# Optimization experiments

Measured on AMD Instinct MI355X. Metric: run time of the kernel, lower is better.

The kernel has to match this reference:

```python
import jax, jax.numpy as jnp
import numpy as np

N, S, T = 32, 256, 256
ENC, H, MEL, PRE, DIN, PN = 512, 256, 80, 128, 64, 512


def setup_inputs():
    key = jax.random.key(0)
    ks = iter(jax.random.split(key, 64))
    def rn(shape, s=0.05):
        return jax.random.normal(next(ks), shape, dtype=jnp.float32) * s
    return dict(
        encoder_outputs=rn((N, S, ENC), 1.0),
        mels=rn((N, MEL, T), 1.0),
        text_lengths=jax.random.randint(next(ks), (N,), 1, S),
        output_lengths=jax.random.randint(next(ks), (N,), 1, T),
        tf_ratio=0,
        enc_Wih=rn((2, 2, 4 * H, ENC)), enc_Whh=rn((2, 2, 4 * H, H)), enc_b=rn((2, 2, 4 * H)),
        Wk=rn((512, 512, 9)), bk=rn((512,)), Wv=rn((512, 512, 9)), bv=rn((512,)),
        Wq=rn((512, 64, 24)), bq=rn((512,)),
        initial_context=rn((1, 1, MEL), 1.0),
        pre_W1=rn((PRE, MEL), 0.1), pre_b1=rn((PRE,)), pre_s1=jnp.ones(PRE, jnp.float32),
        pre_W2=rn((PRE, PRE), 0.1), pre_b2=rn((PRE,)), pre_s2=jnp.ones(PRE, jnp.float32),
        pre_W3=rn((DIN, PRE), 0.1), pre_b3=rn((DIN,)),
        proj_W=rn((DIN, 512)), proj_b=rn((DIN,)),
        gamma=jnp.full((1,), 0.5, jnp.float32),
        dec_Wih0=rn((4 * H, DIN)), dec_Wih_rest=rn((3, 4 * H, H)), dec_Whh=rn((4, 4 * H, H)), dec_b=rn((4, 4 * H)),
        fc_W=rn((MEL, H), 0.1), fc_b=rn((MEL,)),
        stop_W=rn((1, 2 * H), 0.1), stop_b=rn((1,)),
        pn_W0=rn((PN, MEL, 5), 0.1), pn_b0=rn((PN,)),
        pn_Wmid=rn((3, PN, PN, 5)), pn_bmid=rn((3, PN)),
        pn_W4=rn((MEL, PN, 5)), pn_b4=rn((MEL,)),
        pn_bn_scale=jnp.ones((4, PN), jnp.float32), pn_bn_bias=jnp.zeros((4, PN), jnp.float32),
        pn_bn_scale_out=jnp.ones((MEL,), jnp.float32), pn_bn_bias_out=jnp.zeros((MEL,), jnp.float32),
        psine_w=jnp.ones((4, PN), jnp.float32),
    )


def _lstm_scan(xs, Wih, Whh, b, reverse=False):
    # xs: [T, N, D]; torch gate order (i, f, g, o); b = b_ih + b_hh combined
    n = xs.shape[1]
    h0 = jnp.zeros((n, Whh.shape[1]), xs.dtype)
    def step(carry, x):
        h, c = carry
        i, f, g, o = jnp.split(x @ Wih.T + h @ Whh.T + b, 4, axis=-1)
        c = jax.nn.sigmoid(f) * c + jax.nn.sigmoid(i) * jnp.tanh(g)
        h = jax.nn.sigmoid(o) * jnp.tanh(c)
        return (h, c), h
    (h, c), ys = jax.lax.scan(step, (h0, h0), xs, reverse=reverse)
    return ys, h, c


def _conv1d(x, w, b, pad):
    y = jax.lax.conv_general_dilated(x, w, (1,), [pad], dimension_numbers=('NCH', 'OIH', 'NCH'))
    return y + b[None, :, None]


def reference(encoder_outputs, mels, text_lengths, output_lengths, tf_ratio,
              enc_Wih, enc_Whh, enc_b, Wk, bk, Wv, bv, Wq, bq, initial_context,
              pre_W1, pre_b1, pre_s1, pre_W2, pre_b2, pre_s2, pre_W3, pre_b3,
              proj_W, proj_b, gamma, dec_Wih0, dec_Wih_rest, dec_Whh, dec_b,
              fc_W, fc_b, stop_W, stop_b, pn_W0, pn_b0, pn_Wmid, pn_bmid,
              pn_W4, pn_b4, pn_bn_scale, pn_bn_bias, pn_bn_scale_out, pn_bn_bias_out, psine_w):
    # ---- bidirectional 2-layer encoder LSTM ----
    x = encoder_outputs.transpose(1, 0, 2)  # [S, N, ENC]
    hs, cs = [], []
    for l in range(2):
        yf, hf, cf = _lstm_scan(x, enc_Wih[l, 0], enc_Whh[l, 0], enc_b[l, 0])
        yb, hb, cb = _lstm_scan(x, enc_Wih[l, 1], enc_Whh[l, 1], enc_b[l, 1], reverse=True)
        x = jnp.concatenate([yf, yb], -1)
        hs += [hf, hb]; cs += [cf, cb]
    h0 = jnp.stack(hs); c0 = jnp.stack(cs)      # [4, N, H]  (l0f,l0b,l1f,l1b)
    enc_fwd_hidden = hs[2]                       # hidden[-2] = layer1 forward
    enc_nct = x.transpose(1, 2, 0)               # [N, 512, S]
    # ---- K/V conv attention map ----
    k = _conv1d(enc_nct, Wk, bk, (0, 0))         # [N, 512, S-8]
    v = _conv1d(enc_nct, Wv, bv, (0, 0))
    a = jax.nn.softmax(jnp.einsum('nck,ndk->ncd', k, v), axis=-1)  # [N, 512, 512]
    # ---- teacher-forced inputs (tf_ratio == 0 -> rand(1) > 0 always) ----
    mels_ntc = mels.transpose(0, 2, 1)           # [N, T, MEL]
    nb, nt = mels_ntc.shape[0], mels_ntc.shape[1]
    teacher = jnp.concatenate([jnp.tile(initial_context, (nb, 1, 1)), mels_ntc], 1)[:, :nt]
    # prenet (eval: dropout off); PSine: sin(x) * w
    p = jnp.sin(teacher @ pre_W1.T + pre_b1) * pre_s1
    p = jnp.sin(p @ pre_W2.T + pre_b2) * pre_s2
    context = p @ pre_W3.T + pre_b3              # [N, T, 64]
    # ---- growing-context Q conv: at step i, output position i of the
    # kernel-24 pad-12 conv over context[:, :i+1] only involves kernel taps
    # 0..12 (taps 13..23 index positions > i which are zero padding), so it
    # equals a causal conv with the first 13 taps and left pad 12. ----
    q = _conv1d(context.transpose(0, 2, 1), Wq[:, :, :13], bq, (12, 0))  # [N, 512, T]
    o = jnp.einsum('ncd,ndt->ntc', a, q)         # [N, T, 512]
    dec_in = context + gamma * (o @ proj_W.T + proj_b)  # [N, T, 64]
    # ---- 4-layer decoder LSTM (eval: inter-layer dropout off) ----
    def dec_step(carry, xt):
        h, c = carry
        inp = xt
        nh, nc = [], []
        for l in range(4):
            Wih = dec_Wih0 if l == 0 else dec_Wih_rest[l - 1]
            i, f, g, oo = jnp.split(inp @ Wih.T + h[l] @ dec_Whh[l].T + dec_b[l], 4, axis=-1)
            cl = jax.nn.sigmoid(f) * c[l] + jax.nn.sigmoid(i) * jnp.tanh(g)
            hl = jax.nn.sigmoid(oo) * jnp.tanh(cl)
            nh.append(hl); nc.append(cl); inp = hl
        return (jnp.stack(nh), jnp.stack(nc)), inp
    _, top = jax.lax.scan(dec_step, (h0, c0), dec_in.transpose(1, 0, 2))  # [T, N, H]
    outputs = (top @ fc_W.T + fc_b).transpose(1, 2, 0)                    # [N, MEL, T]
    stop_in = jnp.concatenate([top, jnp.broadcast_to(enc_fwd_hidden, top.shape)], -1)
    stop_tokens = (stop_in @ stop_W.T + stop_b).transpose(1, 0, 2)        # [N, T, 1]
    # ---- postnet (eval: BN is per-channel affine, dropout off) ----
    y = _conv1d(outputs, pn_W0, pn_b0, (2, 2))
    y = jnp.sin(y * pn_bn_scale[0][None, :, None] + pn_bn_bias[0][None, :, None]) * psine_w[0][None, :, None]
    for i in range(3):
        y = _conv1d(y, pn_Wmid[i], pn_bmid[i], (2, 2))
        y = jnp.sin(y * pn_bn_scale[i + 1][None, :, None] + pn_bn_bias[i + 1][None, :, None]) * psine_w[i + 1][None, :, None]
    y = _conv1d(y, pn_W4, pn_b4, (2, 2))
    y = y * pn_bn_scale_out[None, :, None] + pn_bn_bias_out[None, :, None]
    post_preds = y + outputs
    return (outputs, post_preds, stop_tokens)
```

## Files before the change

kernel.cpp:

```cpp
#include <hip/hip_runtime.h>
#include <hip/hip_bf16.h>

typedef __hip_bfloat16 bf16;
#define DEV __device__ __forceinline__

typedef __attribute__((ext_vector_type(8))) short bfrag;
typedef __attribute__((ext_vector_type(4))) float facc;

#define PG_    0L
#define ABUF_  0L
#define DPG0_  8388608L
#define Y0_    16777216L
#define ENCT_  18874368L
#define KB_    20975872L
#define VB_    23073024L
#define ABF_   25170176L
#define TEA_   29364480L
#define P1_    29757696L
#define P2_    30281984L
#define CTXP_  30806272L
#define CTXL_  31080704L
#define QB_    31342848L
#define OB_    33440000L
#define DIN_   35537152L
#define TOP_   35799296L
#define OUTF_  36847872L
#define OUTT_  37503232L
#define PN1_   37902592L
#define PN2_   40032512L
#define WKT_   42162432L
#define WVT_   43342080L
#define WQT_   44521728L
#define W1P_   44734720L
#define PN0T_  44740864L
#define PNMT_  44863744L
#define PN4T_  46829824L
#define HDEC_  46964992L
#define HFIN_  47030528L
#define CFIN_  47063296L
#define FLAG_  47096320L
#define CVT_   47096336L
#define WS_NEED_BYTES (52092992L * 4L)

DEV float b2f(bf16 x) { return __bfloat162float(x); }
DEV bf16  f2b(float x) { return __float2bfloat16(x); }
DEV float flo(unsigned v) { union { unsigned u; float f; } c; c.u = v << 16; return c.f; }
DEV float fhi(unsigned v) { union { unsigned u; float f; } c; c.u = v & 0xffff0000u; return c.f; }
DEV unsigned bu(bf16 x) { union { bf16 b; unsigned short u; } c; c.b = x; return (unsigned)c.u; }
DEV unsigned pk2(float a, float b) { return bu(f2b(a)) | (bu(f2b(b)) << 16); }
DEV float sigm(float x) { return 1.0f / (1.0f + __expf(-x)); }

DEV void spin_ge(unsigned* f, unsigned tgt) {
  while (__hip_atomic_load(f, __ATOMIC_RELAXED, __HIP_MEMORY_SCOPE_AGENT) < tgt)
    __builtin_amdgcn_s_sleep(1);
}

DEV void acc8(float& a, uint4 w, const float* x) {
  a += flo(w.x) * x[0] + fhi(w.x) * x[1] + flo(w.y) * x[2] + fhi(w.y) * x[3]
     + flo(w.z) * x[4] + fhi(w.z) * x[5] + flo(w.w) * x[6] + fhi(w.w) * x[7];
}

__global__ void k_flag(const unsigned short* psw, unsigned* flag) {
  if (threadIdx.x == 0 && blockIdx.x == 0) *flag = (psw[0] != 0) ? 1u : 0u;
}

__global__ void k_cvt(const void* src, bf16* dst, long n, const unsigned* flag) {
  long i = (long)blockIdx.x * 256 + threadIdx.x;
  const long stride = (long)gridDim.x * 256;
  if (*flag) {
    const bf16* s = (const bf16*)src;
    for (; i < n; i += stride) dst[i] = s[i];
  } else {
    const float* s = (const float*)src;
    for (; i < n; i += stride) dst[i] = f2b(s[i]);
  }
}

enum { ACT_NONE = 0, ACT_BIAS = 1, ACT_PSINE = 2, ACT_POSTNET = 3, ACT_DECIN = 4, ACT_RESADD = 5 };
enum { SM_F32 = 0, SM_BF16 = 1, SM_PADROW = 2, SM_NCT = 3, SM_TNF32 = 4, SM_RESOUT = 5 };

struct GP {
  const bf16* A; const bf16* B;
  long az, bz, btap;
  int M, N, K, taps;
  int rshift, rpitch;
  float* Cf; bf16* Cb;
  long cz; int cld;
  int p2, pad2, tmax, tp;
  const bf16* bias; long biasz;
  const bf16* s1; const bf16* s2; const bf16* s3;
  const bf16* aux; int auxld;
  const bf16* gamma; const float* res;
};

template<int SM, int ACTM>
__global__ __launch_bounds__(256) void k_gemm(GP p) {
  __shared__ bf16 As[64][40];
  __shared__ bf16 Bs[64][40];
  const int tid = threadIdx.x;
  const int z = blockIdx.z;
  const bf16* Ab = p.A + (long)z * p.az;
  const bf16* Bb = p.B + (long)z * p.bz;
  const int m0 = blockIdx.x * 64, c0 = blockIdx.y * 64;
  const int w = tid >> 6, l = tid & 63;
  const int lrow = tid & 63, lk = (tid >> 6) * 8;
  facc acc[4];
  #pragma unroll
  for (int s = 0; s < 4; ++s) acc[s] = facc{0.f, 0.f, 0.f, 0.f};
  const int am = m0 + lrow;
  const int grp = am >> p.rshift;
  const long arowbase = (long)grp * p.rpitch + (am - (grp << p.rshift));
  const int brow = c0 + lrow;
  const bool bok = brow < p.N;
  const int arow_f = w * 16 + (l & 15);
  const int kf = (l >> 4) * 8;
  for (int j = 0; j < p.taps; ++j) {
    const bf16* Aj = Ab + (arowbase + j) * (long)p.K + lk;
    const bf16* Bj = Bb + (long)j * p.btap + (long)brow * p.K + lk;
    for (int k0 = 0; k0 < p.K; k0 += 32) {
      __syncthreads();
      {
        uint4 av = *(const uint4*)(Aj + k0);
        *(uint4*)&As[lrow][lk] = av;
        uint4 bvv; bvv.x = bvv.y = bvv.z = bvv.w = 0u;
        if (bok) bvv = *(const uint4*)(Bj + k0);
        *(uint4*)&Bs[lrow][lk] = bvv;
      }
      __syncthreads();
      bfrag af = *(const bfrag*)&As[arow_f][kf];
      #pragma unroll
      for (int s = 0; s < 4; ++s) {
        bfrag bf = *(const bfrag*)&Bs[s * 16 + (l & 15)][kf];
        acc[s] = __builtin_amdgcn_mfma_f32_16x16x32_bf16(af, bf, acc[s], 0, 0, 0);
      }
    }
  }
  float gf = 0.f;
  if constexpr (ACTM == ACT_DECIN) gf = b2f(p.gamma[0]);
  #pragma unroll
  for (int s = 0; s < 4; ++s) {
    const int c = c0 + s * 16 + (l & 15);
    if (c >= p.N) continue;
    #pragma unroll
    for (int i = 0; i < 4; ++i) {
      const int m = m0 + w * 16 + ((l >> 4) << 2) + i;
      const int n_ = m >> 8, t_ = m & 255;
      float x = acc[s][i];
      if constexpr (ACTM == ACT_BIAS) x += b2f(p.bias[(long)z * p.biasz + c]);
      else if constexpr (ACTM == ACT_PSINE) x = sinf(x + b2f(p.bias[c])) * b2f(p.s1[c]);
      else if constexpr (ACTM == ACT_POSTNET) x = sinf((x + b2f(p.bias[c])) * b2f(p.s1[c]) + b2f(p.s2[c])) * b2f(p.s3[c]);
      else if constexpr (ACTM == ACT_DECIN) x = b2f(p.aux[(long)m * p.auxld + c]) + gf * (x + b2f(p.bias[c]));
      else if constexpr (ACTM == ACT_RESADD) x = (x + b2f(p.bias[c])) * b2f(p.s1[c]) + b2f(p.s2[c]);
      if constexpr (SM == SM_F32) p.Cf[(long)z * p.cz + (long)m * p.cld + c] = x;
      else if constexpr (SM == SM_BF16) p.Cb[(long)z * p.cz + (long)m * p.cld + c] = f2b(x);
      else if constexpr (SM == SM_PADROW) p.Cb[((long)n_ * p.p2 + p.pad2 + t_) * (long)p.cld + c] = f2b(x);
      else if constexpr (SM == SM_NCT) { if (t_ < p.tmax) p.Cb[((long)n_ * p.p2 + c) * (long)p.tp + t_] = f2b(x); }
      else if constexpr (SM == SM_TNF32) { const int nn = m & 31, tt = m >> 5; p.Cf[((long)nn * p.p2 + c) * (long)p.tp + tt] = x; }
      else if constexpr (SM == SM_RESOUT) { const long off = ((long)n_ * p.p2 + c) * (long)p.tp + t_; p.Cf[off] = x + p.res[off]; }
    }
  }
}

__global__ void k_wtr2(const bf16* __restrict__ in, bf16* __restrict__ out) {
  long i = (long)blockIdx.x * 256 + threadIdx.x;
  if (i >= 524288L) return;
  int jj = (int)(i & 7);
  int r = (int)((i >> 3) & 1023);
  int k8 = (int)((i >> 13) & 31);
  int d = (int)(i >> 18);
  out[i] = in[((long)d * 1024 + r) * 256 + k8 * 8 + jj];
}

__global__ __launch_bounds__(256) void k_enc_scan(
    const float* __restrict__ pg,
    const bf16* __restrict__ WT,
    bf16* __restrict__ ycat,
    float* __restrict__ hfin, float* __restrict__ cfin,
    int layer)
{
  __shared__ float Hs[2][256];
  const int u = threadIdx.x;
  const int d = (int)(blockIdx.x >> 5);
  const int n = (int)(blockIdx.x & 31);
  const bf16* Wd = WT + (long)d * 32 * 1024 * 8;
  const float* pgn = pg + (long)(d * 32 + n) * 256 * 1024;
  float cst = 0.f;
  Hs[0][u] = 0.f;
  __syncthreads();
  for (int it = 0; it < 256; ++it) {
    const int s = d ? (255 - it) : it;
    const int par = it & 1;
    const float* pgs = pgn + (long)s * 1024;
    float a0 = pgs[u], a1 = pgs[256 + u], a2 = pgs[512 + u], a3 = pgs[768 + u];
    #pragma unroll 2
    for (int k8 = 0; k8 < 32; ++k8) {
      float x[8];
      *(float4*)&x[0] = *(const float4*)&Hs[par][k8 * 8];
      *(float4*)&x[4] = *(const float4*)&Hs[par][k8 * 8 + 4];
      const bf16* wb = Wd + ((long)k8 * 1024 + u) * 8;
      acc8(a0, *(const uint4*)(wb), x);
      acc8(a1, *(const uint4*)(wb + 2048), x);
      acc8(a2, *(const uint4*)(wb + 4096), x);
      acc8(a3, *(const uint4*)(wb + 6144), x);
    }
    cst = sigm(a1) * cst + sigm(a0) * tanhf(a2);
    float h = sigm(a3) * tanhf(cst);
    Hs[par ^ 1][u] = h;
    ycat[((long)n * 256 + s) * 512 + d * 256 + u] = f2b(h);
    if (it == 255) {
      hfin[((long)(layer * 2 + d) * 32 + n) * 256 + u] = h;
      cfin[((long)(layer * 2 + d) * 32 + n) * 256 + u] = cst;
    }
    __syncthreads();
  }
}

__global__ __launch_bounds__(256) void k_dec_scan(
    const float* __restrict__ dpg0,
    const bf16* __restrict__ Wih_rest,
    const bf16* __restrict__ Whh,
    const bf16* __restrict__ dec_b,
    unsigned* __restrict__ hdec,
    const float* __restrict__ cfin,
    bf16* __restrict__ top,
    unsigned* __restrict__ flags)
{
  unsigned* gflag = flags + 256 * 32;
  const int tid = threadIdx.x;
  if (blockIdx.x == 256) {
    if (tid < 64) {
      for (int target = 1; target <= 259; ++target) {
        for (;;) {
          unsigned mn = 0xffffffffu;
          #pragma unroll
          for (int q = 0; q < 4; ++q) {
            unsigned v = __hip_atomic_load(&flags[(tid * 4 + q) * 32],
                                           __ATOMIC_RELAXED, __HIP_MEMORY_SCOPE_AGENT);
            mn = mn < v ? mn : v;
          }
          if (__all(mn >= (unsigned)target)) break;
          __builtin_amdgcn_s_sleep(1);
        }
        if (tid < 8)
          __hip_atomic_store(&gflag[tid * 64], (unsigned)target,
                             __ATOMIC_RELAXED, __HIP_MEMORY_SCOPE_AGENT);
      }
    }
    return;
  }
  __shared__ bf16 Wl[16][520];
  __shared__ bf16 XH[32][536];
  __shared__ float Gs[16 * 33];
  __shared__ float Hst[128];
  const int layer = (int)(blockIdx.x >> 6);
  const int g = (int)(blockIdx.x & 63);
  const int u0 = g * 4;
  const int kstart = (layer == 0) ? 256 : 0;
  {
    const int r = tid >> 4, seg = tid & 15;
    const int grow = (r >> 2) * 256 + u0 + (r & 3);
    const int kk = seg * 32;
    const bool part0 = kk < 256;
    if (!(part0 && layer == 0)) {
      const bf16* wp = part0
          ? (Wih_rest + ((long)(layer - 1) * 1024 + grow) * 256 + kk)
          : (Whh + ((long)layer * 1024 + grow) * 256 + (kk - 256));
      for (int q = 0; q < 32; q += 8) {
        uint4 v = *(const uint4*)(wp + q);
        *(uint4*)&Wl[r][kk + q] = v;
      }
    }
  }
  const int pn = tid >> 2, pu = tid & 3;
  float cst = 0.f, bi0 = 0.f, bi1 = 0.f, bi2 = 0.f, bi3 = 0.f;
  if (tid < 128) {
    cst = cfin[((long)layer * 32 + pn) * 256 + u0 + pu];
    if (layer > 0) {
      bi0 = b2f(dec_b[layer * 1024 + u0 + pu]);
      bi1 = b2f(dec_b[layer * 1024 + 256 + u0 + pu]);
      bi2 = b2f(dec_b[layer * 1024 + 512 + u0 + pu]);
      bi3 = b2f(dec_b[layer * 1024 + 768 + u0 + pu]);
    }
  }
  __syncthreads();
  unsigned* myflag = &flags[blockIdx.x * 32];
  unsigned* mygf = &gflag[(blockIdx.x & 7) * 64];
  for (int R = 0; R < 259; ++R) {
    if (R > 0) {
      if (tid == 0) spin_ge(mygf, (unsigned)R);
      __syncthreads();
    }
    const int t = R - layer;
    if (t >= 0 && t < 256) {
      const int rp = (R + 1) & 1, wpar = R & 1;
      {
        const int n = tid >> 3, seg = tid & 7;
        if (layer > 0 || seg >= 4) {
          const unsigned* src = (seg < 4)
              ? (hdec + (((long)(layer - 1) * 2 + rp) * 32 + n) * 128 + seg * 32)
              : (hdec + (((long)layer * 2 + rp) * 32 + n) * 128 + (seg - 4) * 32);
          const int base = seg * 64;
          #pragma unroll
          for (int q = 0; q < 32; q += 4) {
            unsigned long long v01 = __hip_atomic_load((const unsigned long long*)(src + q),
                                                       __ATOMIC_RELAXED, __HIP_MEMORY_SCOPE_AGENT);
            unsigned long long v23 = __hip_atomic_load((const unsigned long long*)(src + q + 2),
                                                       __ATOMIC_RELAXED, __HIP_MEMORY_SCOPE_AGENT);
            *(uint4*)&XH[n][base + q * 2] =
                make_uint4((unsigned)v01, (unsigned)(v01 >> 32), (unsigned)v23, (unsigned)(v23 >> 32));
          }
        }
      }
      __syncthreads();
      {
        const int r = tid & 15, n0 = (tid >> 4) * 2;
        float a0 = 0, a1 = 0;
        const bf16* wr = &Wl[r][0];
        const bf16* xa = &XH[n0][0];
        const bf16* xb = &XH[n0 + 1][0];
        #pragma unroll 4
        for (int k = kstart; k < 512; k += 4) {
          uint2 wv = *(const uint2*)(wr + k);
          uint2 va = *(const uint2*)(xa + k);
          uint2 vb = *(const uint2*)(xb + k);
          float w0 = flo(wv.x), w1 = fhi(wv.x), w2 = flo(wv.y), w3 = fhi(wv.y);
          a0 += w0 * flo(va.x) + w1 * fhi(va.x) + w2 * flo(va.y) + w3 * fhi(va.y);
          a1 += w0 * flo(vb.x) + w1 * fhi(vb.x) + w2 * flo(vb.y) + w3 * fhi(vb.y);
        }
        Gs[r * 33 + n0] = a0;
        Gs[r * 33 + n0 + 1] = a1;
      }
      __syncthreads();
      if (tid < 128) {
        float g0 = Gs[(0 * 4 + pu) * 33 + pn] + bi0;
        float g1 = Gs[(1 * 4 + pu) * 33 + pn] + bi1;
        float g2 = Gs[(2 * 4 + pu) * 33 + pn] + bi2;
        float g3 = Gs[(3 * 4 + pu) * 33 + pn] + bi3;
        if (layer == 0) {
          const float* pp = dpg0 + ((long)pn * 256 + t) * 1024;
          g0 += pp[u0 + pu]; g1 += pp[256 + u0 + pu];
          g2 += pp[512 + u0 + pu]; g3 += pp[768 + u0 + pu];
        }
        cst = sigm(g1) * cst + sigm(g0) * tanhf(g2);
        float h = sigm(g3) * tanhf(cst);
        Hst[tid] = h;
        if (layer == 3) top[((long)t * 32 + pn) * 256 + u0 + pu] = f2b(h);
      }
      __syncthreads();
      if (tid < 64) {
        const int hn = tid >> 1, pr = tid & 1;
        unsigned v = pk2(Hst[hn * 4 + pr * 2], Hst[hn * 4 + pr * 2 + 1]);
        __hip_atomic_store(&hdec[(((long)layer * 2 + wpar) * 32 + hn) * 128 + (u0 >> 1) + pr], v,
                           __ATOMIC_RELAXED, __HIP_MEMORY_SCOPE_AGENT);
      }
      asm volatile("s_waitcnt vmcnt(0)" ::: "memory");
    }
    __syncthreads();
    if (tid == 0)
      __hip_atomic_store(myflag, (unsigned)(R + 1),
                         __ATOMIC_RELAXED, __HIP_MEMORY_SCOPE_AGENT);
  }
}

__global__ void k_wtr(const void* __restrict__ in, bf16* __restrict__ out,
                      int Cout, int Cin, int Cpad, int taps, int tstride, long total,
                      const unsigned* __restrict__ flag) {
  long i = (long)blockIdx.x * 256 + threadIdx.x;
  if (i >= total) return;
  int ci = (int)(i % Cpad); long r = i / Cpad; int co = (int)(r % Cout); int j = (int)(r / Cout);
  float v = 0.f;
  if (ci < Cin) {
    long idx = ((long)co * Cin + ci) * tstride + j;
    v = (*flag) ? b2f(((const bf16*)in)[idx]) : ((const float*)in)[idx];
  }
  out[i] = f2b(v);
}

__global__ void k_softmax(const float* __restrict__ raw, bf16* __restrict__ out) {
  __shared__ float red[256];
  const long row = blockIdx.x;
  const float* r = raw + row * 512;
  const int tid = threadIdx.x;
  float a = r[tid], b = r[tid + 256];
  red[tid] = fmaxf(a, b);
  __syncthreads();
  for (int s = 128; s > 0; s >>= 1) { if (tid < s) red[tid] = fmaxf(red[tid], red[tid + s]); __syncthreads(); }
  const float m = red[0];
  __syncthreads();
  float e0 = __expf(a - m), e1 = __expf(b - m);
  red[tid] = e0 + e1;
  __syncthreads();
  for (int s = 128; s > 0; s >>= 1) { if (tid < s) red[tid] += red[tid + s]; __syncthreads(); }
  const float inv = 1.f / red[0];
  out[row * 512 + tid] = f2b(e0 * inv);
  out[row * 512 + tid + 256] = f2b(e1 * inv);
}

__global__ void k_teacher(const bf16* __restrict__ mels, const bf16* __restrict__ ictx, bf16* __restrict__ out) {
  long i = (long)blockIdx.x * 256 + threadIdx.x;
  if (i >= 8192L * 96) return;
  int c = (int)(i % 96); long m = i / 96; int n = (int)(m >> 8), t = (int)(m & 255);
  float v = 0.f;
  if (c < 80) v = (t == 0) ? b2f(ictx[c]) : b2f(mels[((long)n * 80 + c) * 256 + (t - 1)]);
  out[i] = f2b(v);
}

__global__ void k_ctxcopy(const bf16* __restrict__ ctxp, bf16* __restrict__ ctxl) {
  long i = (long)blockIdx.x * 256 + threadIdx.x;
  if (i >= 8192L * 64) return;
  int c = (int)(i & 63); long m = i >> 6; int n = (int)(m >> 8), t = (int)(m & 255);
  ctxl[i] = ctxp[((long)n * 268 + 12 + t) * 64 + c];
}

__global__ void k_hdec_init(const float* __restrict__ hfin, unsigned* __restrict__ hdec) {
  int i = blockIdx.x * 256 + threadIdx.x;
  if (i >= 16384) return;
  int l = i >> 12, r = i & 4095;
  unsigned v = pk2(hfin[(long)l * 8192 + r * 2], hfin[(long)l * 8192 + r * 2 + 1]);
  hdec[((long)l * 2 + 0) * 4096 + r] = v;
  hdec[((long)l * 2 + 1) * 4096 + r] = v;
}

__global__ void k_outcopy1(const float* __restrict__ of, float* __restrict__ o) {
  long i = (long)blockIdx.x * 256 + threadIdx.x;
  if (i < 655360L) o[i] = of[i];
}

__global__ void k_outcopy2(const float* __restrict__ of, bf16* __restrict__ ot) {
  long i = (long)blockIdx.x * 256 + threadIdx.x;
  if (i >= 655360L) return;
  int c = (int)(i % 80); long m = i / 80; int n = (int)(m >> 8), t = (int)(m & 255);
  ot[((long)n * 260 + 2 + t) * 96 + c] = f2b(of[((long)n * 80 + c) * 256 + t]);
}

__global__ void k_stop(const bf16* __restrict__ top, const float* __restrict__ hfin,
                       const bf16* __restrict__ sW, const bf16* __restrict__ sb, float* __restrict__ out) {
  int i = blockIdx.x * 256 + threadIdx.x;
  if (i >= 8192) return;
  int n = i >> 8, t = i & 255;
  float acc = b2f(sb[0]);
  const bf16* tr = top + ((long)t * 32 + n) * 256;
  for (int h = 0; h < 256; ++h) acc += b2f(tr[h]) * b2f(sW[h]);
  const float* er = hfin + ((long)2 * 32 + n) * 256;
  for (int h = 0; h < 256; ++h) acc += er[h] * b2f(sW[256 + h]);
  out[(long)n * 256 + t] = acc;
}

extern "C" void kernel_launch(void* const* d_in, const int* in_sizes, int n_in,
                              void* d_out, int out_size, void* d_ws, size_t ws_size,
                              hipStream_t stream) {
  (void)in_sizes; (void)n_in; (void)out_size;
  if (ws_size < (size_t)WS_NEED_BYTES) return;

  float* ws = (float*)d_ws;
  float* out0 = (float*)d_out;
  float* out1 = out0 + 655360L;
  float* out2 = out0 + 1310720L;
  #define WF(off) (ws + (off))
  #define WB(off) ((bf16*)(ws + (off)))
  unsigned* flagp = (unsigned*)WF(FLAG_);

  hipMemsetAsync(WF(ENCT_), 0, 2101248L * 4, stream);
  hipMemsetAsync(WF(KB_), 0, 2097152L * 4, stream);
  hipMemsetAsync(WF(VB_), 0, 2097152L * 4, stream);
  hipMemsetAsync(WF(CTXP_), 0, 274432L * 4, stream);
  hipMemsetAsync(WF(OUTT_), 0, 399360L * 4, stream);

  k_flag<<<dim3(1), dim3(64), 0, stream>>>((const unsigned short*)d_in[44], flagp);
  bf16* cv[48] = {};
  {
    struct CvtEnt { int idx; long n; };
    static const CvtEnt cvts[] = {
      {0, 4194304}, {1, 655360}, {5, 2097152}, {6, 1048576}, {7, 4096},
      {9, 512}, {11, 512}, {13, 512}, {14, 80},
      {16, 128}, {17, 128}, {18, 16384}, {19, 128}, {20, 128}, {21, 8192}, {22, 64},
      {23, 32768}, {24, 64}, {25, 1},
      {26, 65536}, {27, 786432}, {28, 1048576}, {29, 4096},
      {30, 20480}, {31, 80}, {32, 512}, {33, 1},
      {35, 512}, {37, 1536}, {39, 80},
      {40, 2048}, {41, 2048}, {42, 80}, {43, 80}, {44, 2048},
    };
    bf16* arena = WB(CVT_);
    long pos = 0;
    for (const auto& c : cvts) {
      bf16* dst = arena + pos;
      long g = (c.n + 255) / 256; if (g > 2048) g = 2048;
      k_cvt<<<dim3((unsigned)g), dim3(256), 0, stream>>>(d_in[c.idx], dst, c.n, flagp);
      cv[c.idx] = dst;
      pos += (c.n + 15) & ~15L;
    }
  }

  const bf16* enc_out = cv[0];
  const bf16* mels    = cv[1];
  const bf16* eWih    = cv[5];
  const bf16* eWhh    = cv[6];
  const bf16* eb      = cv[7];
  const bf16* bk      = cv[9];
  const bf16* bv      = cv[11];
  const bf16* bq      = cv[13];
  const bf16* ictx    = cv[14];
  const bf16* pb1     = cv[16];
  const bf16* ps1     = cv[17];
  const bf16* pW2     = cv[18];
  const bf16* pb2     = cv[19];
  const bf16* ps2     = cv[20];
  const bf16* pW3     = cv[21];
  const bf16* pb3     = cv[22];
  const bf16* prW     = cv[23];
  const bf16* prb     = cv[24];
  const bf16* gam     = cv[25];
  const bf16* dWih0   = cv[26];
  const bf16* dWihr   = cv[27];
  const bf16* dWhh    = cv[28];
  const bf16* db      = cv[29];
  const bf16* fcW     = cv[30];
  const bf16* fcb     = cv[31];
  const bf16* sW      = cv[32];
  const bf16* sb      = cv[33];
  const bf16* pnb0    = cv[35];
  const bf16* pnbm    = cv[37];
  const bf16* pnb4    = cv[39];
  const bf16* bns     = cv[40];
  const bf16* bnb     = cv[41];
  const bf16* bnso    = cv[42];
  const bf16* bnbo    = cv[43];

  auto tr = [&](const void* in, bf16* o, int Cout, int Cin, int Cpad, int to, int ts) {
    long tot = (long)to * Cout * Cpad;
    k_wtr<<<dim3((unsigned)((tot + 255) / 256)), dim3(256), 0, stream>>>(in, o, Cout, Cin, Cpad, to, ts, tot, flagp);
  };
  tr(d_in[8],  WB(WKT_), 512, 512, 512, 9, 9);
  tr(d_in[10], WB(WVT_), 512, 512, 512, 9, 9);
  tr(d_in[12], WB(WQT_), 512, 64, 64, 13, 24);
  tr(d_in[15], WB(W1P_), 128, 80, 96, 1, 1);
  tr(d_in[34], WB(PN0T_), 512, 80, 96, 5, 5);
  tr(d_in[36], WB(PNMT_), 1536, 512, 512, 5, 5);
  tr(d_in[38], WB(PN4T_), 80, 512, 512, 5, 5);

  {
    GP p{}; p.A = enc_out; p.az = 0; p.rshift = 8; p.rpitch = 256;
    p.B = eWih; p.bz = 1024L * 512; p.btap = 0;
    p.M = 8192; p.N = 1024; p.K = 512; p.taps = 1;
    p.Cf = WF(PG_); p.cz = 8388608; p.cld = 1024; p.bias = eb; p.biasz = 1024;
    k_gemm<SM_F32, ACT_BIAS><<<dim3(128, 16, 2), dim3(256), 0, stream>>>(p);
  }
  k_wtr2<<<dim3(2048), dim3(256), 0, stream>>>(eWhh, WB(PN1_));
  k_enc_scan<<<dim3(64), dim3(256), 0, stream>>>(
      WF(PG_), WB(PN1_), WB(Y0_), WF(HFIN_), WF(CFIN_), 0);
  {
    GP p{}; p.A = WB(Y0_); p.az = 0; p.rshift = 8; p.rpitch = 256;
    p.B = eWih + 2L * 1024 * 512; p.bz = 1024L * 512; p.btap = 0;
    p.M = 8192; p.N = 1024; p.K = 512; p.taps = 1;
    p.Cf = WF(PG_); p.cz = 8388608; p.cld = 1024; p.bias = eb + 2048; p.biasz = 1024;
    k_gemm<SM_F32, ACT_BIAS><<<dim3(128, 16, 2), dim3(256), 0, stream>>>(p);
  }
  k_wtr2<<<dim3(2048), dim3(256), 0, stream>>>(eWhh + 2L * 1024 * 256, WB(PN2_));
  k_enc_scan<<<dim3(64), dim3(256), 0, stream>>>(
      WF(PG_), WB(PN2_), WB(ENCT_), WF(HFIN_), WF(CFIN_), 1);
  hipMemsetAsync(WF(PN1_), 0, 2129920L * 4, stream);
  hipMemsetAsync(WF(PN2_), 0, 2129920L * 4, stream);

  for (int kv = 0; kv < 2; ++kv) {
    GP p{}; p.A = WB(ENCT_); p.az = 0; p.rshift = 8; p.rpitch = 256;
    p.B = kv ? WB(WVT_) : WB(WKT_); p.bz = 0; p.btap = 512L * 512;
    p.M = 8192; p.N = 512; p.K = 512; p.taps = 9;
    p.Cb = kv ? WB(VB_) : WB(KB_); p.cz = 0; p.cld = 512;
    p.p2 = 512; p.tp = 256; p.tmax = 248; p.bias = kv ? bv : bk; p.biasz = 0;
    k_gemm<SM_NCT, ACT_BIAS><<<dim3(128, 8, 1), dim3(256), 0, stream>>>(p);
  }
  {
    GP p{}; p.A = WB(KB_); p.az = 512L * 256; p.rshift = 9; p.rpitch = 512;
    p.B = WB(VB_); p.bz = 512L * 256; p.btap = 0;
    p.M = 512; p.N = 512; p.K = 256; p.taps = 1;
    p.Cf = WF(ABUF_); p.cz = 262144; p.cld = 512;
    k_gemm<SM_F32, ACT_NONE><<<dim3(8, 8, 32), dim3(256), 0, stream>>>(p);
  }
  k_softmax<<<dim3(16384), dim3(256), 0, stream>>>(WF(ABUF_), WB(ABF_));

  k_teacher<<<dim3(3072), dim3(256), 0, stream>>>(mels, ictx, WB(TEA_));
  {
    GP p{}; p.A = WB(TEA_); p.az = 0; p.rshift = 8; p.rpitch = 256;
    p.B = WB(W1P_); p.bz = 0; p.btap = 0;
    p.M = 8192; p.N = 128; p.K = 96; p.taps = 1;
    p.Cb = WB(P1_); p.cz = 0; p.cld = 128; p.bias = pb1; p.s1 = ps1;
    k_gemm<SM_BF16, ACT_PSINE><<<dim3(128, 2, 1), dim3(256), 0, stream>>>(p);
  }
  {
    GP p{}; p.A = WB(P1_); p.az = 0; p.rshift = 8; p.rpitch = 256;
    p.B = pW2; p.bz = 0; p.btap = 0;
    p.M = 8192; p.N = 128; p.K = 128; p.taps = 1;
    p.Cb = WB(P2_); p.cz = 0; p.cld = 128; p.bias = pb2; p.s1 = ps2;
    k_gemm<SM_BF16, ACT_PSINE><<<dim3(128, 2, 1), dim3(256), 0, stream>>>(p);
  }
  {
    GP p{}; p.A = WB(P2_); p.az = 0; p.rshift = 8; p.rpitch = 256;
    p.B = pW3; p.bz = 0; p.btap = 0;
    p.M = 8192; p.N = 64; p.K = 128; p.taps = 1;
    p.Cb = WB(CTXP_); p.cz = 0; p.cld = 64; p.p2 = 268; p.pad2 = 12; p.bias = pb3; p.biasz = 0;
    k_gemm<SM_PADROW, ACT_BIAS><<<dim3(128, 1, 1), dim3(256), 0, stream>>>(p);
  }
  k_ctxcopy<<<dim3(2048), dim3(256), 0, stream>>>(WB(CTXP_), WB(CTXL_));

  {
    GP p{}; p.A = WB(CTXP_); p.az = 0; p.rshift = 8; p.rpitch = 268;
    p.B = WB(WQT_); p.bz = 0; p.btap = 512L * 64;
    p.M = 8192; p.N = 512; p.K = 64; p.taps = 13;
    p.Cb = WB(QB_); p.cz = 0; p.cld = 512; p.bias = bq; p.biasz = 0;
    k_gemm<SM_BF16, ACT_BIAS><<<dim3(128, 8, 1), dim3(256), 0, stream>>>(p);
  }
  {
    GP p{}; p.A = WB(QB_); p.az = 256L * 512; p.rshift = 8; p.rpitch = 256;
    p.B = WB(ABF_); p.bz = 512L * 512; p.btap = 0;
    p.M = 256; p.N = 512; p.K = 512; p.taps = 1;
    p.Cb = WB(OB_); p.cz = 256L * 512; p.cld = 512;
    k_gemm<SM_BF16, ACT_NONE><<<dim3(4, 8, 32), dim3(256), 0, stream>>>(p);
  }
  {
    GP p{}; p.A = WB(OB_); p.az = 0; p.rshift = 8; p.rpitch = 256;
    p.B = prW; p.bz = 0; p.btap = 0;
    p.M = 8192; p.N = 64; p.K = 512; p.taps = 1;
    p.Cb = WB(DIN_); p.cz = 0; p.cld = 64;
    p.bias = prb; p.aux = WB(CTXL_); p.auxld = 64; p.gamma = gam;
    k_gemm<SM_BF16, ACT_DECIN><<<dim3(128, 1, 1), dim3(256), 0, stream>>>(p);
  }
  {
    GP p{}; p.A = WB(DIN_); p.az = 0; p.rshift = 8; p.rpitch = 256;
    p.B = dWih0; p.bz = 0; p.btap = 0;
    p.M = 8192; p.N = 1024; p.K = 64; p.taps = 1;
    p.Cf = WF(DPG0_); p.cz = 0; p.cld = 1024; p.bias = db; p.biasz = 0;
    k_gemm<SM_F32, ACT_BIAS><<<dim3(128, 16, 1), dim3(256), 0, stream>>>(p);
  }
  hipMemsetAsync(WF(ABUF_), 0, 40960, stream);
  k_hdec_init<<<dim3(64), dim3(256), 0, stream>>>(WF(HFIN_), (unsigned*)WF(HDEC_));
  k_dec_scan<<<dim3(257), dim3(256), 0, stream>>>(
      WF(DPG0_), dWihr, dWhh, db, (unsigned*)WF(HDEC_), WF(CFIN_), WB(TOP_), (unsigned*)WF(ABUF_));

  {
    GP p{}; p.A = WB(TOP_); p.az = 0; p.rshift = 8; p.rpitch = 256;
    p.B = fcW; p.bz = 0; p.btap = 0;
    p.M = 8192; p.N = 80; p.K = 256; p.taps = 1;
    p.Cf = WF(OUTF_); p.p2 = 80; p.tp = 256; p.bias = fcb; p.biasz = 0;
    k_gemm<SM_TNF32, ACT_BIAS><<<dim3(128, 2, 1), dim3(256), 0, stream>>>(p);
  }
  k_outcopy1<<<dim3(2560), dim3(256), 0, stream>>>(WF(OUTF_), out0);
  k_outcopy2<<<dim3(2560), dim3(256), 0, stream>>>(WF(OUTF_), WB(OUTT_));
  k_stop<<<dim3(32), dim3(256), 0, stream>>>(WB(TOP_), WF(HFIN_), sW, sb, out2);

  {
    GP p{}; p.A = WB(OUTT_); p.az = 0; p.rshift = 8; p.rpitch = 260;
    p.B = WB(PN0T_); p.bz = 0; p.btap = 512L * 96;
    p.M = 8192; p.N = 512; p.K = 96; p.taps = 5;
    p.Cb = WB(PN1_); p.cz = 0; p.cld = 512; p.p2 = 260; p.pad2 = 2;
    p.bias = pnb0; p.s1 = bns; p.s2 = bnb; p.s3 = cv[44];
    k_gemm<SM_PADROW, ACT_POSTNET><<<dim3(128, 8, 1), dim3(256), 0, stream>>>(p);
  }
  for (int s3 = 0; s3 < 3; ++s3) {
    GP p{}; p.A = (s3 & 1) ? WB(PN2_) : WB(PN1_); p.az = 0; p.rshift = 8; p.rpitch = 260;
    p.B = WB(PNMT_) + (long)s3 * 512 * 512; p.bz = 0; p.btap = 1536L * 512;
    p.M = 8192; p.N = 512; p.K = 512; p.taps = 5;
    p.Cb = (s3 & 1) ? WB(PN1_) : WB(PN2_); p.cz = 0; p.cld = 512; p.p2 = 260; p.pad2 = 2;
    p.bias = pnbm + s3 * 512; p.s1 = bns + (s3 + 1) * 512; p.s2 = bnb + (s3 + 1) * 512; p.s3 = cv[44] + (s3 + 1) * 512;
    k_gemm<SM_PADROW, ACT_POSTNET><<<dim3(128, 8, 1), dim3(256), 0, stream>>>(p);
  }
  {
    GP p{}; p.A = WB(PN2_); p.az = 0; p.rshift = 8; p.rpitch = 260;
    p.B = WB(PN4T_); p.bz = 0; p.btap = 80L * 512;
    p.M = 8192; p.N = 80; p.K = 512; p.taps = 5;
    p.Cf = out1; p.p2 = 80; p.tp = 256;
    p.bias = pnb4; p.s1 = bnso; p.s2 = bnbo; p.res = WF(OUTF_);
    k_gemm<SM_RESOUT, ACT_RESADD><<<dim3(128, 2, 1), dim3(256), 0, stream>>>(p);
  }
}
```

Before: 7.782 ms.

## Pack four batch rows per encoder scan block and vectorize decoder h loads

Result: slower. 14.70 ms, median of 2 (+89.0%).

```diff
diff --git a/kernel.cpp b/kernel.cpp
--- a/kernel.cpp
+++ b/kernel.cpp
@@ -171,32 +171,33 @@
   out[i] = in[((long)d * 1024 + r) * 256 + k8 * 8 + jj];
 }
 
-__global__ __launch_bounds__(256) void k_enc_scan(
+__global__ __launch_bounds__(1024) void k_enc_scan(
     const float* __restrict__ pg,
     const bf16* __restrict__ WT,
     bf16* __restrict__ ycat,
     float* __restrict__ hfin, float* __restrict__ cfin,
     int layer)
 {
-  __shared__ float Hs[2][256];
-  const int u = threadIdx.x;
-  const int d = (int)(blockIdx.x >> 5);
-  const int n = (int)(blockIdx.x & 31);
+  __shared__ float Hs[2][4][256];
+  const int tid = threadIdx.x;
+  const int u = tid & 255, nl = tid >> 8;
+  const int d = (int)(blockIdx.x >> 3);
+  const int n = ((int)blockIdx.x & 7) * 4 + nl;
   const bf16* Wd = WT + (long)d * 32 * 1024 * 8;
   const float* pgn = pg + (long)(d * 32 + n) * 256 * 1024;
   float cst = 0.f;
-  Hs[0][u] = 0.f;
+  Hs[0][nl][u] = 0.f;
   __syncthreads();
   for (int it = 0; it < 256; ++it) {
     const int s = d ? (255 - it) : it;
     const int par = it & 1;
     const float* pgs = pgn + (long)s * 1024;
     float a0 = pgs[u], a1 = pgs[256 + u], a2 = pgs[512 + u], a3 = pgs[768 + u];
-    #pragma unroll 2
+    #pragma unroll 4
     for (int k8 = 0; k8 < 32; ++k8) {
       float x[8];
-      *(float4*)&x[0] = *(const float4*)&Hs[par][k8 * 8];
-      *(float4*)&x[4] = *(const float4*)&Hs[par][k8 * 8 + 4];
+      *(float4*)&x[0] = *(const float4*)&Hs[par][nl][k8 * 8];
+      *(float4*)&x[4] = *(const float4*)&Hs[par][nl][k8 * 8 + 4];
       const bf16* wb = Wd + ((long)k8 * 1024 + u) * 8;
       acc8(a0, *(const uint4*)(wb), x);
       acc8(a1, *(const uint4*)(wb + 2048), x);
@@ -205,7 +206,7 @@
     }
     cst = sigm(a1) * cst + sigm(a0) * tanhf(a2);
     float h = sigm(a3) * tanhf(cst);
-    Hs[par ^ 1][u] = h;
+    Hs[par ^ 1][nl][u] = h;
     ycat[((long)n * 256 + s) * 512 + d * 256 + u] = f2b(h);
     if (it == 255) {
       hfin[((long)(layer * 2 + d) * 32 + n) * 256 + u] = h;
@@ -292,23 +293,17 @@
     }
     const int t = R - layer;
     if (t >= 0 && t < 256) {
+      __builtin_amdgcn_fence(__ATOMIC_ACQUIRE, "agent");
       const int rp = (R + 1) & 1, wpar = R & 1;
       {
         const int n = tid >> 3, seg = tid & 7;
         if (layer > 0 || seg >= 4) {
-          const unsigned* src = (seg < 4)
-              ? (hdec + (((long)(layer - 1) * 2 + rp) * 32 + n) * 128 + seg * 32)
-              : (hdec + (((long)layer * 2 + rp) * 32 + n) * 128 + (seg - 4) * 32);
-          const int base = seg * 64;
+          const uint4* src = (seg < 4)
+              ? (const uint4*)(hdec + (((long)(layer - 1) * 2 + rp) * 32 + n) * 128 + seg * 32)
+              : (const uint4*)(hdec + (((long)layer * 2 + rp) * 32 + n) * 128 + (seg - 4) * 32);
+          uint4* dst = (uint4*)&XH[n][seg * 64];
           #pragma unroll
-          for (int q = 0; q < 32; q += 4) {
-            unsigned long long v01 = __hip_atomic_load((const unsigned long long*)(src + q),
-                                                       __ATOMIC_RELAXED, __HIP_MEMORY_SCOPE_AGENT);
-            unsigned long long v23 = __hip_atomic_load((const unsigned long long*)(src + q + 2),
-                                                       __ATOMIC_RELAXED, __HIP_MEMORY_SCOPE_AGENT);
-            *(uint4*)&XH[n][base + q * 2] =
-                make_uint4((unsigned)v01, (unsigned)(v01 >> 32), (unsigned)v23, (unsigned)(v23 >> 32));
-          }
+          for (int q = 0; q < 8; ++q) dst[q] = src[q];
         }
       }
       __syncthreads();
@@ -546,7 +541,7 @@
     k_gemm<SM_F32, ACT_BIAS><<<dim3(128, 16, 2), dim3(256), 0, stream>>>(p);
   }
   k_wtr2<<<dim3(2048), dim3(256), 0, stream>>>(eWhh, WB(PN1_));
-  k_enc_scan<<<dim3(64), dim3(256), 0, stream>>>(
+  k_enc_scan<<<dim3(16), dim3(1024), 0, stream>>>(
       WF(PG_), WB(PN1_), WB(Y0_), WF(HFIN_), WF(CFIN_), 0);
   {
     GP p{}; p.A = WB(Y0_); p.az = 0; p.rshift = 8; p.rpitch = 256;
@@ -556,7 +551,7 @@
     k_gemm<SM_F32, ACT_BIAS><<<dim3(128, 16, 2), dim3(256), 0, stream>>>(p);
   }
   k_wtr2<<<dim3(2048), dim3(256), 0, stream>>>(eWhh + 2L * 1024 * 256, WB(PN2_));
-  k_enc_scan<<<dim3(64), dim3(256), 0, stream>>>(
+  k_enc_scan<<<dim3(16), dim3(1024), 0, stream>>>(
       WF(PG_), WB(PN2_), WB(ENCT_), WF(HFIN_), WF(CFIN_), 1);
   hipMemsetAsync(WF(PN1_), 0, 2129920L * 4, stream);
   hipMemsetAsync(WF(PN2_), 0, 2129920L * 4, stream);
```
